# Optimization experiments

Hardware: AMD Instinct MI355X
Metric: run time of the kernel (lower is better)

## Reference

```python
import jax, jax.numpy as jnp
import numpy as np

DIM = 1024
HEADS = 16
HEAD_DIM = DIM // HEADS
RPE_K = 16
B, T = 4, 1024


def setup_inputs() -> dict:
    key = jax.random.key(0)
    ks = jax.random.split(key, 12)
    s = 1.0 / np.sqrt(DIM)
    inp = {
        'q': jax.random.normal(ks[0], (B, T, DIM), jnp.float32),
        'k': jax.random.normal(ks[1], (B, T, DIM), jnp.float32),
        'v': jax.random.normal(ks[2], (B, T, DIM), jnp.float32),
        'Wq': jax.random.normal(ks[3], (DIM, DIM), jnp.float32) * s,
        'bq': jnp.zeros((DIM,), jnp.float32),
        'Wk': jax.random.normal(ks[4], (DIM, DIM), jnp.float32) * s,
        'bk': jnp.zeros((DIM,), jnp.float32),
        'Wv': jax.random.normal(ks[5], (DIM, DIM), jnp.float32) * s,
        'bv': jnp.zeros((DIM,), jnp.float32),
        'rpe_w': jax.random.normal(ks[6], (2 * RPE_K + 1, 2 * HEAD_DIM), jnp.float32) * 0.02,
        'Wo': jax.random.normal(ks[7], (DIM, DIM), jnp.float32) * s,
        'bo': jnp.zeros((DIM,), jnp.float32),
    }
    return inp


def reference(q, k, v, Wq, bq, Wk, bk, Wv, bv, rpe_w, Wo, bo):
    b, ql = q.shape[:2]
    kl = k.shape[1]
    split = lambda x: x.reshape(b, -1, HEADS, HEAD_DIM).transpose(0, 2, 1, 3)  # b h t d
    qh = split(q @ Wq.T + bq)
    kh = split(k @ Wk.T + bk)
    vh = split(v @ Wv.T + bv)
    # note: original scales q BEFORE both the k-dot and the rpe_q einsum
    qh = qh / np.sqrt(HEAD_DIM)
    # relative distance table (constant ints)
    idx = jnp.arange(max(ql, kl))
    dist = jnp.clip(idx[:, None] - idx[None, :], -RPE_K, RPE_K) + RPE_K
    dist = dist[:ql, :kl]
    rpe = rpe_w[dist]                      # (ql, kl, 2*HEAD_DIM)
    rpe_q, rpe_v = jnp.split(rpe, 2, axis=-1)
    energy = jnp.einsum('bhqd,bhkd->bhqk', qh, kh)
    energy = energy + jnp.einsum('bhqd,qkd->bhqk', qh, rpe_q)
    alignment = jax.nn.softmax(energy, axis=-1)
    context = jnp.einsum('bhqk,bhkd->bhqd', alignment, vh)
    context = context + jnp.einsum('bhqk,qkd->bhqd', alignment, rpe_v)
    context = context.transpose(0, 2, 1, 3).reshape(b, ql, DIM)
    out = context @ Wo.T + bo
    return (out, alignment)
```

## Files before the change

kernel.cpp:

```cpp
#include <hip/hip_runtime.h>
#include <stdint.h>

typedef unsigned short u16;
typedef unsigned int   u32;
typedef short bf16x8 __attribute__((ext_vector_type(8)));
typedef float floatx4 __attribute__((ext_vector_type(4)));

#define OFF_XQ   0u
#define OFF_XK   4194304u
#define OFF_XV   8388608u
#define OFF_WQ   12582912u
#define OFF_WK   13631488u
#define OFF_WV   14680064u
#define OFF_WO   15728640u
#define OFF_QH   16777216u
#define OFF_KH   20971520u
#define OFF_VT   25165824u
#define OFF_CTX  29360128u

__device__ __forceinline__ u16 f2b(float f){
  u32 u = __float_as_uint(f);
  u = (u + 0x7fffu + ((u >> 16) & 1u)) >> 16;
  return (u16)u;
}
__device__ __forceinline__ float b2f(u16 h){
  return __uint_as_float(((u32)h) << 16);
}

__global__ __launch_bounds__(256) void convert_kernel(
    const float* __restrict__ q, const float* __restrict__ k, const float* __restrict__ v,
    const float* __restrict__ Wq, const float* __restrict__ Wk, const float* __restrict__ Wv,
    const float* __restrict__ Wo, u16* __restrict__ ws){
  int y = blockIdx.y;
  const float* src; u16* dst; int n;
  switch(y){
    case 0: src=q;  dst=ws+OFF_XQ; n=4194304; break;
    case 1: src=k;  dst=ws+OFF_XK; n=4194304; break;
    case 2: src=v;  dst=ws+OFF_XV; n=4194304; break;
    case 3: src=Wq; dst=ws+OFF_WQ; n=1048576; break;
    case 4: src=Wk; dst=ws+OFF_WK; n=1048576; break;
    case 5: src=Wv; dst=ws+OFF_WV; n=1048576; break;
    default:src=Wo; dst=ws+OFF_WO; n=1048576; break;
  }
  int idx = (blockIdx.x*256 + threadIdx.x)*4;
  if (idx >= n) return;
  float4 f = *(const float4*)(src + idx);
  ushort4 o;
  o.x = f2b(f.x); o.y = f2b(f.y); o.z = f2b(f.z); o.w = f2b(f.w);
  *(ushort4*)(dst + idx) = o;
}

template<int MODE>
__global__ __launch_bounds__(256) void gemm_kernel(
    const u16* __restrict__ A0, const u16* __restrict__ B0,
    const float* __restrict__ b0, const float* __restrict__ b1, const float* __restrict__ b2,
    u16* __restrict__ ws, float* __restrict__ outF){
  constexpr int BN = (MODE==0) ? 128 : 64;
  constexpr int NJ = BN/32;
  __shared__ u16 As[128][32];
  __shared__ u16 Bs[BN][32];
  int z = (MODE==0) ? blockIdx.z : 0;
  const u16* A  = A0 + (size_t)z*4194304u;
  const u16* Bm = B0 + (size_t)z*1048576u;
  const float* bias = (MODE==0) ? (z==0?b0:b1) : b0;
  int tid  = threadIdx.x;
  int lane = tid & 63, wave = tid >> 6;
  int wm = (wave>>1)*64, wn = (wave&1)*(BN/2);
  int m_base = blockIdx.y*128, n_base = blockIdx.x*BN;
  floatx4 acc[4][NJ] = {};
  int fr = lane & 15, fo = (lane>>4)*8;
  int srow = lane >> 2, sseg = (lane & 3)*8;
  u16* AsW0 = &As[wave*32][0];
  u16* AsW1 = &As[wave*32+16][0];
  const u16* Ag0 = A  + (size_t)(m_base + wave*32      + srow)*1024 + sseg;
  const u16* Ag1 = A  + (size_t)(m_base + wave*32 + 16 + srow)*1024 + sseg;
  u16* BsW0; u16* BsW1; const u16* Bg0; const u16* Bg1;
  if constexpr (BN==128){
    BsW0 = &Bs[wave*32][0];    BsW1 = &Bs[wave*32+16][0];
    Bg0 = Bm + (size_t)(n_base + wave*32      + srow)*1024 + sseg;
    Bg1 = Bm + (size_t)(n_base + wave*32 + 16 + srow)*1024 + sseg;
  } else {
    BsW0 = &Bs[wave*16][0];    BsW1 = nullptr;
    Bg0 = Bm + (size_t)(n_base + wave*16 + srow)*1024 + sseg;
    Bg1 = nullptr;
  }
  for (int kb = 0; kb < 1024; kb += 32){
    __builtin_amdgcn_global_load_lds((const u32*)(Ag0 + kb), (u32*)AsW0, 16, 0, 0);
    __builtin_amdgcn_global_load_lds((const u32*)(Ag1 + kb), (u32*)AsW1, 16, 0, 0);
    __builtin_amdgcn_global_load_lds((const u32*)(Bg0 + kb), (u32*)BsW0, 16, 0, 0);
    if constexpr (BN==128)
      __builtin_amdgcn_global_load_lds((const u32*)(Bg1 + kb), (u32*)BsW1, 16, 0, 0);
    __syncthreads();
    bf16x8 af[4], bfr[NJ];
    #pragma unroll
    for (int i=0;i<4;i++)
      af[i]  = *(const bf16x8*)(&As[wm + i*16 + fr][fo]);
    #pragma unroll
    for (int j=0;j<NJ;j++)
      bfr[j] = *(const bf16x8*)(&Bs[wn + j*16 + fr][fo]);
    #pragma unroll
    for (int i=0;i<4;i++)
      #pragma unroll
      for (int j=0;j<NJ;j++)
        acc[i][j] = __builtin_amdgcn_mfma_f32_16x16x32_bf16(af[i], bfr[j], acc[i][j], 0,0,0);
    __syncthreads();
  }
  int col = lane & 15, rb = (lane>>4)*4;
  #pragma unroll
  for (int i=0;i<4;i++){
    #pragma unroll
    for (int j=0;j<NJ;j++){
      int nn = n_base + wn + j*16 + col;
      float bvn = (MODE==2) ? 0.f : bias[nn];
      #pragma unroll
      for (int r=0;r<4;r++){
        int mm = m_base + wm + i*16 + rb + r;
        if constexpr (MODE==0){
          float v = acc[i][j][r] + bvn;
          if (z==0) v *= 0.125f;
          int b = mm>>10, t = mm&1023, h = nn>>6, d = nn&63;
          u32 base = (z==0)?OFF_QH:OFF_KH;
          u32 idx = (((u32)(b*16+h))<<16) + ((u32)(t<<6)) + (u32)d;
          ws[base + idx] = f2b(v);
        } else if constexpr (MODE==1){
          outF[(size_t)mm*1024 + nn] = acc[i][j][r] + bvn;
        } else {
          float v = acc[i][j][r] + bias[mm];
          int h = mm>>6, d = mm&63, b = nn>>10, t = nn&1023;
          u32 idx = (((u32)(b*16+h))<<16) + ((u32)(d<<10)) + (u32)t;
          ws[OFF_VT + idx] = f2b(v);
        }
      }
    }
  }
}

__global__ __launch_bounds__(256) void attn_kernel(
    const u16* __restrict__ ws, const float* __restrict__ rpe_w,
    float* __restrict__ d_out, u16* __restrict__ ctx){
  __shared__ u16   P[16][1032];
  __shared__ u16   qs[16][64];
  __shared__ float proj[16][33];
  __shared__ float sacc[16][3];
  __shared__ float slds[16][33];
  __shared__ float linv[16];

  int bid = blockIdx.x;
  int qt = bid & 63, bh = bid >> 6;
  int q0 = qt * 16;
  int tid = threadIdx.x, lane = tid & 63, wave = tid >> 6;

  const u16* qh = ws + OFF_QH + (size_t)bh*65536;
  const u16* kh = ws + OFF_KH + (size_t)bh*65536;
  const u16* vT = ws + OFF_VT + (size_t)bh*65536;

  if (tid < 128){
    int r = tid >> 3, c = (tid & 7)*8;
    *(uint4*)(&qs[r][c]) = *(const uint4*)(qh + (size_t)(q0+r)*64 + c);
  }
  if (tid < 48) ((float*)sacc)[tid] = 0.f;
  __syncthreads();

  for (int i = tid; i < 16*33; i += 256){
    int r = i / 33, t = i - r*33;
    float s = 0.f;
    #pragma unroll
    for (int d=0; d<64; d++) s += b2f(qs[r][d]) * rpe_w[t*128 + d];
    proj[r][t] = s;
  }
  __syncthreads();

  int col = lane & 15, rb = (lane>>4)*4, fo = (lane>>4)*8;
  bf16x8 aq0 = *(const bf16x8*)(&qs[col][fo]);
  bf16x8 aq1 = *(const bf16x8*)(&qs[col][32 + fo]);

  float tot[4] = {0,0,0,0}, lo[4] = {0,0,0,0}, hi[4] = {0,0,0,0};
  for (int kb = 0; kb < 1024; kb += 64){
    int key = kb + wave*16 + col;
    const u16* kp = kh + (size_t)key*64 + fo;
    bf16x8 bk0 = *(const bf16x8*)(kp);
    bf16x8 bk1 = *(const bf16x8*)(kp + 32);
    floatx4 s4 = {0.f,0.f,0.f,0.f};
    s4 = __builtin_amdgcn_mfma_f32_16x16x32_bf16(aq0, bk0, s4, 0,0,0);
    s4 = __builtin_amdgcn_mfma_f32_16x16x32_bf16(aq1, bk1, s4, 0,0,0);
    #pragma unroll
    for (int r=0;r<4;r++){
      int row = rb + r;
      int qg = q0 + row;
      int dd = qg - key;
      int bkt = min(max(dd, -16), 16) + 16;
      float p = __expf(s4[r] + proj[row][bkt]);
      P[row][key] = f2b(p);
      tot[r] += p;
      if      (key <= qg - 16) lo[r] += p;
      else if (key >= qg + 16) hi[r] += p;
    }
  }
  #pragma unroll
  for (int r=0;r<4;r++){
    #pragma unroll
    for (int m=8;m>=1;m>>=1){
      tot[r] += __shfl_xor(tot[r], m, 16);
      lo[r]  += __shfl_xor(lo[r],  m, 16);
      hi[r]  += __shfl_xor(hi[r],  m, 16);
    }
  }
  if (col == 0){
    #pragma unroll
    for (int r=0;r<4;r++){
      atomicAdd(&sacc[rb+r][0], tot[r]);
      atomicAdd(&sacc[rb+r][1], lo[r]);
      atomicAdd(&sacc[rb+r][2], hi[r]);
    }
  }
  __syncthreads();

  if (tid < 16){
    linv[tid] = 1.f / sacc[tid][0];
    slds[tid][32] = sacc[tid][1];
    slds[tid][0]  = sacc[tid][2];
  }
  for (int i = tid; i < 16*31; i += 256){
    int r = i / 31, t = 1 + (i - r*31);
    int kk = q0 + r + 16 - t;
    slds[r][t] = (kk >= 0 && kk < 1024) ? b2f(P[r][kk]) : 0.f;
  }
  __syncthreads();

  {
    int row = tid >> 4, c0 = (tid & 15)*4;
    float li = linv[row];
    float* outA = d_out + 4194304u + ((size_t)(bh*1024 + q0 + row))*1024;
    #pragma unroll
    for (int i=0;i<16;i++){
      int kcol = c0 + i*64;
      ushort4 pv = *(const ushort4*)(&P[row][kcol]);
      float4 o;
      o.x = b2f(pv.x)*li; o.y = b2f(pv.y)*li;
      o.z = b2f(pv.z)*li; o.w = b2f(pv.w)*li;
      *(float4*)(outA + kcol) = o;
    }
  }

  floatx4 o4 = {0.f,0.f,0.f,0.f};
  int n0 = wave*16;
  {
    const u16* vbase = vT + (size_t)(n0 + col)*1024;
    for (int kk = 0; kk < 1024; kk += 32){
      bf16x8 ap  = *(const bf16x8*)(&P[col][kk + fo]);
      bf16x8 bv8 = *(const bf16x8*)(vbase + kk + fo);
      o4 = __builtin_amdgcn_mfma_f32_16x16x32_bf16(ap, bv8, o4, 0,0,0);
    }
  }
  {
    int b = bh >> 4, h = bh & 15;
    int d = n0 + col;
    float sv[4] = {0.f,0.f,0.f,0.f};
    const float* rv = rpe_w + 64 + d;
    #pragma unroll
    for (int t=0;t<33;t++){
      float rvt = rv[t*128];
      #pragma unroll
      for (int r=0;r<4;r++) sv[r] += slds[rb+r][t]*rvt;
    }
    #pragma unroll
    for (int r=0;r<4;r++){
      int row = rb + r;
      float v = (o4[r] + sv[r]) * linv[row];
      ctx[((size_t)(b*1024 + q0 + row))*1024 + h*64 + d] = f2b(v);
    }
  }
}

extern "C" void kernel_launch(void* const* d_in, const int* in_sizes, int n_in,
                              void* d_out, int out_size, void* d_ws, size_t ws_size,
                              hipStream_t stream){
  const float* q  = (const float*)d_in[0];
  const float* k  = (const float*)d_in[1];
  const float* v  = (const float*)d_in[2];
  const float* Wq = (const float*)d_in[3];
  const float* bq = (const float*)d_in[4];
  const float* Wk = (const float*)d_in[5];
  const float* bk = (const float*)d_in[6];
  const float* Wv = (const float*)d_in[7];
  const float* bv = (const float*)d_in[8];
  const float* rpe= (const float*)d_in[9];
  const float* Wo = (const float*)d_in[10];
  const float* bo = (const float*)d_in[11];
  u16* ws = (u16*)d_ws;
  float* out = (float*)d_out;

  convert_kernel<<<dim3(4096,7), 256, 0, stream>>>(q,k,v,Wq,Wk,Wv,Wo, ws);
  gemm_kernel<0><<<dim3(8,32,2), 256, 0, stream>>>(ws+OFF_XQ, ws+OFF_WQ, bq, bk, nullptr, ws, nullptr);
  gemm_kernel<2><<<dim3(64,8),   256, 0, stream>>>(ws+OFF_WV, ws+OFF_XV, bv, nullptr, nullptr, ws, nullptr);
  attn_kernel<<<dim3(4096), 256, 0, stream>>>(ws, rpe, out, ws+OFF_CTX);
  gemm_kernel<1><<<dim3(16,32), 256, 0, stream>>>(ws+OFF_CTX, ws+OFF_WO, bo, nullptr, nullptr, ws, out);
}
```

Baseline: 579.1 us.

## Merge QKV projections into one launch, compact convert grid, MFMA rpe projection

Compacts the convert grid so no blocks exit idle on the smaller weight tensors. Fuses the Q/K projections and the transposed V projection into a single GEMM launch using 128x64 tiles, which removes one kernel launch and gives more blocks per launch. In the attention kernel, the scalar q·rpe_q projection loop is replaced with two MFMA ops, and shared-memory atomics are replaced by per-wave partial sums. Unroll pragmas are added to the two main attention loops. Smaller N tiles for the Q/K GEMM mean more A-tile reloads.

```diff
diff --git a/kernel.cpp b/kernel.cpp
--- a/kernel.cpp
+++ b/kernel.cpp
@@ -31,19 +31,21 @@
     const float* __restrict__ q, const float* __restrict__ k, const float* __restrict__ v,
     const float* __restrict__ Wq, const float* __restrict__ Wk, const float* __restrict__ Wv,
     const float* __restrict__ Wo, u16* __restrict__ ws){
-  int y = blockIdx.y;
-  const float* src; u16* dst; int n;
+  int bid = blockIdx.x;
+  int y, local;
+  if (bid < 12288){ y = bid >> 12; local = bid & 4095; }
+  else { int t = bid - 12288; y = 3 + (t >> 10); local = t & 1023; }
+  const float* src; u16* dst;
   switch(y){
-    case 0: src=q;  dst=ws+OFF_XQ; n=4194304; break;
-    case 1: src=k;  dst=ws+OFF_XK; n=4194304; break;
-    case 2: src=v;  dst=ws+OFF_XV; n=4194304; break;
-    case 3: src=Wq; dst=ws+OFF_WQ; n=1048576; break;
-    case 4: src=Wk; dst=ws+OFF_WK; n=1048576; break;
-    case 5: src=Wv; dst=ws+OFF_WV; n=1048576; break;
-    default:src=Wo; dst=ws+OFF_WO; n=1048576; break;
-  }
-  int idx = (blockIdx.x*256 + threadIdx.x)*4;
-  if (idx >= n) return;
+    case 0: src=q;  dst=ws+OFF_XQ; break;
+    case 1: src=k;  dst=ws+OFF_XK; break;
+    case 2: src=v;  dst=ws+OFF_XV; break;
+    case 3: src=Wq; dst=ws+OFF_WQ; break;
+    case 4: src=Wk; dst=ws+OFF_WK; break;
+    case 5: src=Wv; dst=ws+OFF_WV; break;
+    default:src=Wo; dst=ws+OFF_WO; break;
+  }
+  int idx = (local*256 + threadIdx.x)*4;
   float4 f = *(const float4*)(src + idx);
   ushort4 o;
   o.x = f2b(f.x); o.y = f2b(f.y); o.z = f2b(f.z); o.w = f2b(f.w);
@@ -55,53 +57,53 @@
     const u16* __restrict__ A0, const u16* __restrict__ B0,
     const float* __restrict__ b0, const float* __restrict__ b1, const float* __restrict__ b2,
     u16* __restrict__ ws, float* __restrict__ outF){
-  constexpr int BN = (MODE==0) ? 128 : 64;
-  constexpr int NJ = BN/32;
   __shared__ u16 As[128][32];
-  __shared__ u16 Bs[BN][32];
+  __shared__ u16 Bs[64][32];
   int z = (MODE==0) ? blockIdx.z : 0;
-  const u16* A  = A0 + (size_t)z*4194304u;
-  const u16* Bm = B0 + (size_t)z*1048576u;
-  const float* bias = (MODE==0) ? (z==0?b0:b1) : b0;
+  const u16* A; const u16* Bm;
+  int m_base, n_base;
+  if constexpr (MODE==0){
+    if (z < 2){
+      A  = ws + (z==0 ? OFF_XQ : OFF_XK);
+      Bm = ws + (z==0 ? OFF_WQ : OFF_WK);
+      m_base = blockIdx.y*128; n_base = blockIdx.x*64;
+    } else {
+      A  = ws + OFF_WV;  Bm = ws + OFF_XV;
+      int flat = blockIdx.y*16 + blockIdx.x;
+      m_base = (flat>>6)*128; n_base = (flat&63)*64;
+    }
+  } else {
+    A = A0; Bm = B0;
+    m_base = blockIdx.y*128; n_base = blockIdx.x*64;
+  }
   int tid  = threadIdx.x;
   int lane = tid & 63, wave = tid >> 6;
-  int wm = (wave>>1)*64, wn = (wave&1)*(BN/2);
-  int m_base = blockIdx.y*128, n_base = blockIdx.x*BN;
-  floatx4 acc[4][NJ] = {};
+  int wm = (wave>>1)*64, wn = (wave&1)*32;
+  floatx4 acc[4][2] = {};
   int fr = lane & 15, fo = (lane>>4)*8;
   int srow = lane >> 2, sseg = (lane & 3)*8;
   u16* AsW0 = &As[wave*32][0];
   u16* AsW1 = &As[wave*32+16][0];
+  u16* BsW0 = &Bs[wave*16][0];
   const u16* Ag0 = A  + (size_t)(m_base + wave*32      + srow)*1024 + sseg;
   const u16* Ag1 = A  + (size_t)(m_base + wave*32 + 16 + srow)*1024 + sseg;
-  u16* BsW0; u16* BsW1; const u16* Bg0; const u16* Bg1;
-  if constexpr (BN==128){
-    BsW0 = &Bs[wave*32][0];    BsW1 = &Bs[wave*32+16][0];
-    Bg0 = Bm + (size_t)(n_base + wave*32      + srow)*1024 + sseg;
-    Bg1 = Bm + (size_t)(n_base + wave*32 + 16 + srow)*1024 + sseg;
-  } else {
-    BsW0 = &Bs[wave*16][0];    BsW1 = nullptr;
-    Bg0 = Bm + (size_t)(n_base + wave*16 + srow)*1024 + sseg;
-    Bg1 = nullptr;
-  }
+  const u16* Bg0 = Bm + (size_t)(n_base + wave*16      + srow)*1024 + sseg;
   for (int kb = 0; kb < 1024; kb += 32){
     __builtin_amdgcn_global_load_lds((const u32*)(Ag0 + kb), (u32*)AsW0, 16, 0, 0);
     __builtin_amdgcn_global_load_lds((const u32*)(Ag1 + kb), (u32*)AsW1, 16, 0, 0);
     __builtin_amdgcn_global_load_lds((const u32*)(Bg0 + kb), (u32*)BsW0, 16, 0, 0);
-    if constexpr (BN==128)
-      __builtin_amdgcn_global_load_lds((const u32*)(Bg1 + kb), (u32*)BsW1, 16, 0, 0);
     __syncthreads();
-    bf16x8 af[4], bfr[NJ];
+    bf16x8 af[4], bfr[2];
     #pragma unroll
     for (int i=0;i<4;i++)
       af[i]  = *(const bf16x8*)(&As[wm + i*16 + fr][fo]);
     #pragma unroll
-    for (int j=0;j<NJ;j++)
+    for (int j=0;j<2;j++)
       bfr[j] = *(const bf16x8*)(&Bs[wn + j*16 + fr][fo]);
     #pragma unroll
     for (int i=0;i<4;i++)
       #pragma unroll
-      for (int j=0;j<NJ;j++)
+      for (int j=0;j<2;j++)
         acc[i][j] = __builtin_amdgcn_mfma_f32_16x16x32_bf16(af[i], bfr[j], acc[i][j], 0,0,0);
     __syncthreads();
   }
@@ -109,26 +111,26 @@
   #pragma unroll
   for (int i=0;i<4;i++){
     #pragma unroll
-    for (int j=0;j<NJ;j++){
+    for (int j=0;j<2;j++){
       int nn = n_base + wn + j*16 + col;
-      float bvn = (MODE==2) ? 0.f : bias[nn];
       #pragma unroll
       for (int r=0;r<4;r++){
         int mm = m_base + wm + i*16 + rb + r;
-        if constexpr (MODE==0){
-          float v = acc[i][j][r] + bvn;
-          if (z==0) v *= 0.125f;
-          int b = mm>>10, t = mm&1023, h = nn>>6, d = nn&63;
-          u32 base = (z==0)?OFF_QH:OFF_KH;
-          u32 idx = (((u32)(b*16+h))<<16) + ((u32)(t<<6)) + (u32)d;
-          ws[base + idx] = f2b(v);
-        } else if constexpr (MODE==1){
-          outF[(size_t)mm*1024 + nn] = acc[i][j][r] + bvn;
+        float v = acc[i][j][r];
+        if constexpr (MODE==1){
+          outF[(size_t)mm*1024 + nn] = v + b0[nn];
         } else {
-          float v = acc[i][j][r] + bias[mm];
-          int h = mm>>6, d = mm&63, b = nn>>10, t = nn&1023;
-          u32 idx = (((u32)(b*16+h))<<16) + ((u32)(d<<10)) + (u32)t;
-          ws[OFF_VT + idx] = f2b(v);
+          if (z < 2){
+            v += (z==0 ? b0 : b1)[nn];
+            if (z==0) v *= 0.125f;
+            int b = mm>>10, t = mm&1023, h = nn>>6, d = nn&63;
+            u32 base = (z==0)?OFF_QH:OFF_KH;
+            ws[base + (((u32)(b*16+h))<<16) + ((u32)(t<<6)) + (u32)d] = f2b(v);
+          } else {
+            v += b2[mm];
+            int h = mm>>6, d = mm&63, b = nn>>10, t = nn&1023;
+            ws[OFF_VT + (((u32)(b*16+h))<<16) + ((u32)(d<<10)) + (u32)t] = f2b(v);
+          }
         }
       }
     }
@@ -141,7 +143,7 @@
   __shared__ u16   P[16][1032];
   __shared__ u16   qs[16][64];
   __shared__ float proj[16][33];
-  __shared__ float sacc[16][3];
+  __shared__ float ssum[4][16][3];
   __shared__ float slds[16][33];
   __shared__ float linv[16];
 
@@ -149,6 +151,7 @@
   int qt = bid & 63, bh = bid >> 6;
   int q0 = qt * 16;
   int tid = threadIdx.x, lane = tid & 63, wave = tid >> 6;
+  int col = lane & 15, rb = (lane>>4)*4, fo = (lane>>4)*8;
 
   const u16* qh = ws + OFF_QH + (size_t)bh*65536;
   const u16* kh = ws + OFF_KH + (size_t)bh*65536;
@@ -158,23 +161,31 @@
     int r = tid >> 3, c = (tid & 7)*8;
     *(uint4*)(&qs[r][c]) = *(const uint4*)(qh + (size_t)(q0+r)*64 + c);
   }
-  if (tid < 48) ((float*)sacc)[tid] = 0.f;
   __syncthreads();
 
-  for (int i = tid; i < 16*33; i += 256){
-    int r = i / 33, t = i - r*33;
-    float s = 0.f;
-    #pragma unroll
-    for (int d=0; d<64; d++) s += b2f(qs[r][d]) * rpe_w[t*128 + d];
-    proj[r][t] = s;
-  }
-  __syncthreads();
-
-  int col = lane & 15, rb = (lane>>4)*4, fo = (lane>>4)*8;
   bf16x8 aq0 = *(const bf16x8*)(&qs[col][fo]);
   bf16x8 aq1 = *(const bf16x8*)(&qs[col][32 + fo]);
 
+  if (wave < 3){
+    int t_r = wave*16 + col;
+    int t_c = min(t_r, 32);
+    const float* rp = rpe_w + t_c*128 + fo;
+    bf16x8 ar0, ar1;
+    #pragma unroll
+    for (int j=0;j<8;j++){ ar0[j] = (short)f2b(rp[j]); ar1[j] = (short)f2b(rp[32+j]); }
+    floatx4 s4 = {0.f,0.f,0.f,0.f};
+    s4 = __builtin_amdgcn_mfma_f32_16x16x32_bf16(ar0, aq0, s4, 0,0,0);
+    s4 = __builtin_amdgcn_mfma_f32_16x16x32_bf16(ar1, aq1, s4, 0,0,0);
+    #pragma unroll
+    for (int r=0;r<4;r++){
+      int t_out = wave*16 + rb + r;
+      if (t_out <= 32) proj[col][t_out] = s4[r];
+    }
+  }
+  __syncthreads();
+
   float tot[4] = {0,0,0,0}, lo[4] = {0,0,0,0}, hi[4] = {0,0,0,0};
+  #pragma unroll 4
   for (int kb = 0; kb < 1024; kb += 64){
     int key = kb + wave*16 + col;
     const u16* kp = kh + (size_t)key*64 + fo;
@@ -208,17 +219,20 @@
   if (col == 0){
     #pragma unroll
     for (int r=0;r<4;r++){
-      atomicAdd(&sacc[rb+r][0], tot[r]);
-      atomicAdd(&sacc[rb+r][1], lo[r]);
-      atomicAdd(&sacc[rb+r][2], hi[r]);
+      ssum[wave][rb+r][0] = tot[r];
+      ssum[wave][rb+r][1] = lo[r];
+      ssum[wave][rb+r][2] = hi[r];
     }
   }
   __syncthreads();
 
   if (tid < 16){
-    linv[tid] = 1.f / sacc[tid][0];
-    slds[tid][32] = sacc[tid][1];
-    slds[tid][0]  = sacc[tid][2];
+    float T = ssum[0][tid][0]+ssum[1][tid][0]+ssum[2][tid][0]+ssum[3][tid][0];
+    float L = ssum[0][tid][1]+ssum[1][tid][1]+ssum[2][tid][1]+ssum[3][tid][1];
+    float H = ssum[0][tid][2]+ssum[1][tid][2]+ssum[2][tid][2]+ssum[3][tid][2];
+    linv[tid] = 1.f / T;
+    slds[tid][32] = L;
+    slds[tid][0]  = H;
   }
   for (int i = tid; i < 16*31; i += 256){
     int r = i / 31, t = 1 + (i - r*31);
@@ -246,6 +260,7 @@
   int n0 = wave*16;
   {
     const u16* vbase = vT + (size_t)(n0 + col)*1024;
+    #pragma unroll 4
     for (int kk = 0; kk < 1024; kk += 32){
       bf16x8 ap  = *(const bf16x8*)(&P[col][kk + fo]);
       bf16x8 bv8 = *(const bf16x8*)(vbase + kk + fo);
@@ -290,9 +305,8 @@
   u16* ws = (u16*)d_ws;
   float* out = (float*)d_out;
 
-  convert_kernel<<<dim3(4096,7), 256, 0, stream>>>(q,k,v,Wq,Wk,Wv,Wo, ws);
-  gemm_kernel<0><<<dim3(8,32,2), 256, 0, stream>>>(ws+OFF_XQ, ws+OFF_WQ, bq, bk, nullptr, ws, nullptr);
-  gemm_kernel<2><<<dim3(64,8),   256, 0, stream>>>(ws+OFF_WV, ws+OFF_XV, bv, nullptr, nullptr, ws, nullptr);
+  convert_kernel<<<dim3(16384), 256, 0, stream>>>(q,k,v,Wq,Wk,Wv,Wo, ws);
+  gemm_kernel<0><<<dim3(16,32,3), 256, 0, stream>>>(nullptr, nullptr, bq, bk, bv, ws, nullptr);
   attn_kernel<<<dim3(4096), 256, 0, stream>>>(ws, rpe, out, ws+OFF_CTX);
   gemm_kernel<1><<<dim3(16,32), 256, 0, stream>>>(ws+OFF_CTX, ws+OFF_WO, bo, nullptr, nullptr, ws, out);
 }
```

Result: faster. 522.6 us (-9.8%).
